# Kernel optimization log

Measured on AMD Instinct MI355X. Metric: run time of the kernel, lower is better.

## Reference

```python
import jax, jax.numpy as jnp
import numpy as np

NUM_USERS = 100000
NUM_ITEMS = 50000
N = NUM_USERS + NUM_ITEMS
E = 3000000
DIM = 64


def setup_inputs() -> dict:
    key = jax.random.key(0)
    ks = jax.random.split(key, 8)
    emb_users = 0.01 * jax.random.normal(ks[0], (NUM_USERS, DIM), dtype=jnp.float32)
    emb_items = 0.01 * jax.random.normal(ks[1], (NUM_ITEMS, DIM), dtype=jnp.float32)
    # GCNConv linear weights (bias separate, as in PyG: lin(bias=False) + bias param)
    s = 1.0 / np.sqrt(DIM)
    W1 = jax.random.uniform(ks[2], (DIM, DIM), jnp.float32, -s, s)
    b1 = jnp.zeros((DIM,), jnp.float32)
    W2 = jax.random.uniform(ks[3], (DIM, DIM), jnp.float32, -s, s)
    b2 = jnp.zeros((DIM,), jnp.float32)
    edge_index = jax.random.randint(ks[4], (2, E), 0, N, dtype=jnp.int64)
    edge_weight = jax.random.uniform(ks[5], (E,), jnp.float32)
    return {"emb_users": emb_users, "emb_items": emb_items,
            "W1": W1, "b1": b1, "W2": W2, "b2": b2,
            "edge_index": edge_index, "edge_weight": edge_weight}


def _gcn_conv(x, W, b, row, col):
    """PyG GCNConv with add_self_loops=True, improved=False, unit edge weights.
    out[i] = sum_{j->i} d_j^-1/2 d_i^-1/2 (x_j W) + d_i^-1 (x_i W) + b
    where d includes the self-loop (+1).
    """
    n = x.shape[0]
    xw = x @ W                                           # [N, D]
    deg = jax.ops.segment_sum(jnp.ones_like(row, dtype=x.dtype), col,
                              num_segments=n) + 1.0      # in-degree + self-loop
    dinv = jax.lax.rsqrt(deg)                            # [N]
    coef = dinv[row] * dinv[col]                         # [E]
    msg = xw[row] * coef[:, None]                        # gather + scale  [E, D]
    out = jax.ops.segment_sum(msg, col, num_segments=n)  # scatter-add     [N, D]
    out = out + xw * (dinv * dinv)[:, None]              # self-loop term
    return out + b


def reference(emb_users, emb_items, W1, b1, W2, b2, edge_index, edge_weight):
    # edge_weight is accepted by forward() but never passed to the GCN convs
    row, col = edge_index[0], edge_index[1]
    emb = jnp.concatenate([emb_users, emb_items], axis=0)  # [N, D]
    embs = [emb]
    for W, b in ((W1, b1), (W2, b2)):
        emb = _gcn_conv(emb, W, b, row, col)
        embs.append(emb)
        emb = jax.nn.relu(emb)
    return jnp.stack(embs)  # [num_layers+1, N, D]
```

## Files before the change

kernel.cpp:

```cpp
#include <hip/hip_runtime.h>
#include <hip/hip_fp16.h>

#define DIM 64
#define BPN 1024
#define ECHUNK 8192
#define MAXNB 160
#define BCAP 22528

typedef _Float16 f16x8 __attribute__((ext_vector_type(8)));
typedef float f32x4 __attribute__((ext_vector_type(4)));


__global__ __launch_bounds__(1024) void count_scatter_kernel(
    const int* __restrict__ row, const int* __restrict__ col,
    int* __restrict__ cursor_rel, int* __restrict__ packed, int E, int NB) {
  __shared__ int h[MAXNB];
  __shared__ int excl0[MAXNB];
  __shared__ int cur[MAXNB];
  __shared__ int gbase[MAXNB];
  __shared__ int wsum[16];
  __shared__ int woff[16];
  __shared__ int staging[ECHUNK];
  __shared__ unsigned short map[ECHUNK];
  const int tid = threadIdx.x;
  for (int t = tid; t < NB; t += blockDim.x) h[t] = 0;
  __syncthreads();
  int base = blockIdx.x * ECHUNK;
  int end = min(base + ECHUNK, E);
  int total = end - base;
  for (int e = base + tid; e < end; e += blockDim.x)
    atomicAdd(&h[col[e] >> 10], 1);
  __syncthreads();
  {
    const int lane = tid & 63, wid = tid >> 6;
    int v = (tid < NB) ? h[tid] : 0;
    int x = v;
#pragma unroll
    for (int d = 1; d < 64; d <<= 1) {
      int s = __shfl_up(x, d, 64);
      if (lane >= d) x += s;
    }
    if (lane == 63) wsum[wid] = x;
    __syncthreads();
    if (tid == 0) {
      int s = 0;
#pragma unroll
      for (int k = 0; k < 16; k++) { woff[k] = s; s += wsum[k]; }
    }
    __syncthreads();
    if (tid < NB) {
      int excl = woff[wid] + x - v;
      excl0[tid] = excl;
      cur[tid] = excl;
    }
  }
  __syncthreads();
  if (tid < NB) {
    if (h[tid] > 0)
      gbase[tid] = tid * BCAP + atomicAdd(&cursor_rel[tid], h[tid]);
    int s = excl0[tid], c = h[tid];
    for (int j = 0; j < c; j++) map[s + j] = (unsigned short)tid;
  }
  __syncthreads();
  for (int e = base + tid; e < end; e += blockDim.x) {
    int c = col[e];
    int b = c >> 10;
    int pos = atomicAdd(&cur[b], 1);
    staging[pos] = ((c & (BPN - 1)) << 18) | row[e];
  }
  __syncthreads();
  for (int idx = tid; idx < total; idx += blockDim.x) {
    int b = map[idx];
    packed[gbase[b] + idx - excl0[b]] = staging[idx];
  }
}

__global__ __launch_bounds__(256) void bucket_scan_kernel(
    const int* __restrict__ bucket_cnt, int* __restrict__ bucket_base,
    int* __restrict__ off, int NB, int N, int E) {
  __shared__ int wsum[4];
  __shared__ int woff[4];
  const int t = threadIdx.x;
  const int lane = t & 63, wid = t >> 6;
  int v = (t < NB) ? bucket_cnt[t] : 0;
  int x = v;
#pragma unroll
  for (int d = 1; d < 64; d <<= 1) {
    int s = __shfl_up(x, d, 64);
    if (lane >= d) x += s;
  }
  if (lane == 63) wsum[wid] = x;
  __syncthreads();
  if (t == 0) {
    int s = 0;
#pragma unroll
    for (int k = 0; k < 4; k++) { woff[k] = s; s += wsum[k]; }
  }
  __syncthreads();
  if (t < NB) bucket_base[t] = woff[wid] + x - v;
  if (t == 0) {
    bucket_base[NB] = woff[3] + wsum[3];
    off[N] = E;
  }
}

__global__ __launch_bounds__(1024) void bucket_csr_kernel(
    const int* __restrict__ packed, const int* __restrict__ bucket_base,
    int* __restrict__ perm_row, int* __restrict__ off, float* __restrict__ dinv, int N) {
  __shared__ int nh[BPN];
  __shared__ int ncur[BPN];
  __shared__ int wsum[16];
  __shared__ int woff[16];
  const int b = blockIdx.x;
  const int tid = threadIdx.x;
  const int rbase = b * BCAP;
  const int ebase = bucket_base[b];
  const int cnt = bucket_base[b + 1] - ebase;
  nh[tid] = 0;
  __syncthreads();
  for (int i = tid; i < cnt; i += 1024)
    atomicAdd(&nh[packed[rbase + i] >> 18], 1);
  __syncthreads();
  const int lane = tid & 63, wid = tid >> 6;
  int v = nh[tid], x = v;
#pragma unroll
  for (int d = 1; d < 64; d <<= 1) {
    int t = __shfl_up(x, d, 64);
    if (lane >= d) x += t;
  }
  if (lane == 63) wsum[wid] = x;
  __syncthreads();
  if (tid == 0) {
    int s = 0;
#pragma unroll
    for (int k = 0; k < 16; k++) { woff[k] = s; s += wsum[k]; }
  }
  __syncthreads();
  int excl = woff[wid] + x - v;
  ncur[tid] = excl;
  int node = b * BPN + tid;
  if (node < N) {
    off[node] = ebase + excl;
    dinv[node] = rsqrtf((float)v + 1.0f);
  }
  __syncthreads();
  for (int i = tid; i < cnt; i += 1024) {
    int p = packed[rbase + i];
    int local = p >> 18;
    int pos = atomicAdd(&ncur[local], 1);
    perm_row[ebase + pos] = p & 0x3FFFF;
  }
}

__global__ __launch_bounds__(256) void edge_coef_kernel(
    const int* __restrict__ perm_row, const float* __restrict__ dinv,
    int2* __restrict__ edata, int E) {
  int e = blockIdx.x * 256 + threadIdx.x;
  if (e >= E) return;
  int r = perm_row[e];
  edata[e] = make_int2(r, __float_as_int(dinv[r]));
}

__global__ __launch_bounds__(256) void xw_mfma_kernel(
    const float* __restrict__ xa, const float* __restrict__ xb,
    const float* __restrict__ W, float* __restrict__ out0,
    __half* __restrict__ xwh, int NU, int N, int do_relu) {
  __shared__ _Float16 Wt[64 * 72];
  for (int t = threadIdx.x; t < 4096; t += 256) {
    int k = t >> 6, n = t & 63;
    Wt[n * 72 + k] = (_Float16)W[t];
  }
  __syncthreads();
  const int lane = threadIdx.x & 63;
  const int wid = threadIdx.x >> 6;
  const int m = lane & 15;
  const int quad = lane >> 4;
  f16x8 bfrag[4][2];
#pragma unroll
  for (int c = 0; c < 4; c++)
#pragma unroll
    for (int s = 0; s < 2; s++)
      bfrag[c][s] = *(const f16x8*)&Wt[(c * 16 + m) * 72 + s * 32 + quad * 8];

  const int rbase = (blockIdx.x * 4 + wid) * 16;
  if (rbase >= N) return;
  const int r = rbase + m;
  const int rr = min(r, N - 1);
  const float* src = (xb == nullptr || rr < NU) ? xa + (size_t)rr * DIM
                                                : xb + (size_t)(rr - NU) * DIM;
  f16x8 afrag[2];
#pragma unroll
  for (int s = 0; s < 2; s++) {
    float4 u0 = *(const float4*)(src + s * 32 + quad * 8);
    float4 u1 = *(const float4*)(src + s * 32 + quad * 8 + 4);
    if (out0 != nullptr && r < N) {
      float4* o = (float4*)(out0 + (size_t)r * DIM);
      o[s * 8 + quad * 2] = u0;
      o[s * 8 + quad * 2 + 1] = u1;
    }
    if (do_relu) {
      u0.x = fmaxf(u0.x, 0.f); u0.y = fmaxf(u0.y, 0.f);
      u0.z = fmaxf(u0.z, 0.f); u0.w = fmaxf(u0.w, 0.f);
      u1.x = fmaxf(u1.x, 0.f); u1.y = fmaxf(u1.y, 0.f);
      u1.z = fmaxf(u1.z, 0.f); u1.w = fmaxf(u1.w, 0.f);
    }
    afrag[s][0] = (_Float16)u0.x; afrag[s][1] = (_Float16)u0.y;
    afrag[s][2] = (_Float16)u0.z; afrag[s][3] = (_Float16)u0.w;
    afrag[s][4] = (_Float16)u1.x; afrag[s][5] = (_Float16)u1.y;
    afrag[s][6] = (_Float16)u1.z; afrag[s][7] = (_Float16)u1.w;
  }
  f32x4 acc[4];
#pragma unroll
  for (int c = 0; c < 4; c++) {
    acc[c] = (f32x4){0.f, 0.f, 0.f, 0.f};
    acc[c] = __builtin_amdgcn_mfma_f32_16x16x32_f16(afrag[0], bfrag[c][0], acc[c], 0, 0, 0);
    acc[c] = __builtin_amdgcn_mfma_f32_16x16x32_f16(afrag[1], bfrag[c][1], acc[c], 0, 0, 0);
  }
#pragma unroll
  for (int reg = 0; reg < 4; reg++) {
    int orow = rbase + quad * 4 + reg;
    if (orow < N) {
      __half* dst = xwh + (size_t)orow * DIM + m;
#pragma unroll
      for (int c = 0; c < 4; c++)
        dst[c * 16] = __float2half(acc[c][reg]);
    }
  }
}

__global__ void aggregate_kernel(const __half* __restrict__ xwh, const int* __restrict__ off,
                                 const int2* __restrict__ edata, const float* __restrict__ dinv,
                                 const float* __restrict__ b, float* __restrict__ out,
                                 int nbase, int ncnt) {
  const int lane = threadIdx.x & 63;
  const int li = blockIdx.x * (blockDim.x >> 6) + (threadIdx.x >> 6);
  if (li >= ncnt) return;
  const int i = nbase + li;
  const int esel = lane >> 3;
  const int j = lane & 7;
  const float di = dinv[i];
  const float4* rows = (const float4*)xwh;
  float acc[8];
#pragma unroll
  for (int q = 0; q < 8; q++) acc[q] = 0.0f;
  if (esel == 0) {
    float4 f = rows[(size_t)i * 8 + j];
    const __half2* h = (const __half2*)&f;
#pragma unroll
    for (int q = 0; q < 4; q++) {
      float2 p = __half22float2(h[q]);
      acc[2 * q] = di * p.x;
      acc[2 * q + 1] = di * p.y;
    }
  }
  const int s0 = off[i], s1 = off[i + 1];
  const int last = s1 - 1;
  for (int k = s0; k < s1; k += 32) {
    const int e0 = k + esel, e1 = e0 + 8, e2 = e0 + 16, e3 = e0 + 24;
    int2 v0 = edata[min(e0, last)];
    int2 v1 = edata[min(e1, last)];
    int2 v2 = edata[min(e2, last)];
    int2 v3 = edata[min(e3, last)];
    float c0 = (e0 <= last) ? __int_as_float(v0.y) : 0.0f;
    float c1 = (e1 <= last) ? __int_as_float(v1.y) : 0.0f;
    float c2 = (e2 <= last) ? __int_as_float(v2.y) : 0.0f;
    float c3 = (e3 <= last) ? __int_as_float(v3.y) : 0.0f;
    float4 f0 = rows[(size_t)v0.x * 8 + j];
    float4 f1 = rows[(size_t)v1.x * 8 + j];
    float4 f2 = rows[(size_t)v2.x * 8 + j];
    float4 f3 = rows[(size_t)v3.x * 8 + j];
    const __half2* h0 = (const __half2*)&f0;
    const __half2* h1 = (const __half2*)&f1;
    const __half2* h2 = (const __half2*)&f2;
    const __half2* h3 = (const __half2*)&f3;
#pragma unroll
    for (int q = 0; q < 4; q++) {
      float2 p0 = __half22float2(h0[q]);
      acc[2 * q] += c0 * p0.x;
      acc[2 * q + 1] += c0 * p0.y;
    }
#pragma unroll
    for (int q = 0; q < 4; q++) {
      float2 p1 = __half22float2(h1[q]);
      acc[2 * q] += c1 * p1.x;
      acc[2 * q + 1] += c1 * p1.y;
    }
#pragma unroll
    for (int q = 0; q < 4; q++) {
      float2 p2 = __half22float2(h2[q]);
      acc[2 * q] += c2 * p2.x;
      acc[2 * q + 1] += c2 * p2.y;
    }
#pragma unroll
    for (int q = 0; q < 4; q++) {
      float2 p3 = __half22float2(h3[q]);
      acc[2 * q] += c3 * p3.x;
      acc[2 * q + 1] += c3 * p3.y;
    }
  }
#pragma unroll
  for (int q = 0; q < 8; q++) {
    acc[q] += __shfl_xor(acc[q], 8, 64);
    acc[q] += __shfl_xor(acc[q], 16, 64);
    acc[q] += __shfl_xor(acc[q], 32, 64);
  }
  if (esel == 0) {
    float4 b0 = ((const float4*)b)[2 * j];
    float4 b1 = ((const float4*)b)[2 * j + 1];
    float4* orow = (float4*)(out + (size_t)i * DIM);
    orow[2 * j] = make_float4(di * acc[0] + b0.x, di * acc[1] + b0.y,
                              di * acc[2] + b0.z, di * acc[3] + b0.w);
    orow[2 * j + 1] = make_float4(di * acc[4] + b1.x, di * acc[5] + b1.y,
                                  di * acc[6] + b1.z, di * acc[7] + b1.w);
  }
}

extern "C" void kernel_launch(void* const* d_in, const int* in_sizes, int n_in,
                              void* d_out, int out_size, void* d_ws, size_t ws_size,
                              hipStream_t stream) {
  const float* emb_users = (const float*)d_in[0];
  const float* emb_items = (const float*)d_in[1];
  const float* W1 = (const float*)d_in[2];
  const float* b1 = (const float*)d_in[3];
  const float* W2 = (const float*)d_in[4];
  const float* b2 = (const float*)d_in[5];
  const int* edge_index = (const int*)d_in[6];

  const int NU = in_sizes[0] / DIM;
  const int NI = in_sizes[1] / DIM;
  const int N = NU + NI;
  const int E = in_sizes[6] / 2;
  const int NB = (N + BPN - 1) / BPN;
  const int* row = edge_index;
  const int* col = edge_index + E;

  float* out = (float*)d_out;

  char* ws = (char*)d_ws;
  size_t o = 0;
  auto alloc = [&](size_t bytes) -> void* {
    o = (o + 255) & ~(size_t)255;
    void* p = ws + o;
    o += bytes;
    return p;
  };
  int* cursor_rel    = (int*)alloc((size_t)NB * 4);
  int* bucket_base   = (int*)alloc((size_t)(NB + 1) * 4);
  int* off           = (int*)alloc((size_t)(N + 1) * 4);
  float* dinv        = (float*)alloc((size_t)N * 4);
  int* perm_row      = (int*)alloc((size_t)E * 4);
  int2* edata        = (int2*)alloc((size_t)E * 8);
  __half* xwh        = (__half*)alloc((size_t)N * DIM * 2);
  int* packed        = (int*)xwh;
  (void)ws_size;

  const int nbE = (E + ECHUNK - 1) / ECHUNK;

  hipMemsetAsync(cursor_rel, 0, (size_t)NB * 4, stream);
  count_scatter_kernel<<<nbE, 1024, 0, stream>>>(row, col, cursor_rel, packed, E, NB);
  bucket_scan_kernel<<<1, 256, 0, stream>>>(cursor_rel, bucket_base, off, NB, N, E);
  bucket_csr_kernel<<<NB, 1024, 0, stream>>>(packed, bucket_base, perm_row, off, dinv, N);
  edge_coef_kernel<<<(E + 255) / 256, 256, 0, stream>>>(perm_row, dinv, edata, E);

  const int TB = 256;
  const int gx = (N + 63) / 64;
  const int NH = (N + 1) / 2;
  const int g1 = (NH + 3) / 4;
  const int g2 = (N - NH + 3) / 4;

  xw_mfma_kernel<<<gx, TB, 0, stream>>>(emb_users, emb_items, W1, out, xwh, NU, N, 0);
  aggregate_kernel<<<g1, TB, 0, stream>>>((const __half*)xwh, off, edata, dinv, b1,
                                          out + (size_t)N * DIM, 0, NH);
  aggregate_kernel<<<g2, TB, 0, stream>>>((const __half*)xwh, off, edata, dinv, b1,
                                          out + (size_t)N * DIM, NH, N - NH);

  xw_mfma_kernel<<<gx, TB, 0, stream>>>(out + (size_t)N * DIM, nullptr, W2, nullptr, xwh, N, N, 1);
  aggregate_kernel<<<g1, TB, 0, stream>>>((const __half*)xwh, off, edata, dinv, b2,
                                          out + (size_t)2 * N * DIM, 0, NH);
  aggregate_kernel<<<g2, TB, 0, stream>>>((const __half*)xwh, off, edata, dinv, b2,
                                          out + (size_t)2 * N * DIM, NH, N - NH);
}
```

Before: 398.6 us.

## Compute degrees in count pass, fuse edge coef into CSR build, merge aggregate launches

Degrees are now accumulated with global atomics during the count/scatter pass, and a small kernel turns them into dinv before CSR construction. The CSR kernel then writes the (row, dinv[row]) pair straight into edata, which removes the perm_row buffer and the separate edge_coef pass over E edges. The two half-range aggregate launches per layer become one launch each. The cost is 3M global atomics on deg and an extra small kernel plus memset size.

```diff
diff --git a/kernel.cpp b/kernel.cpp
--- a/kernel.cpp
+++ b/kernel.cpp
@@ -13,7 +13,8 @@
 
 __global__ __launch_bounds__(1024) void count_scatter_kernel(
     const int* __restrict__ row, const int* __restrict__ col,
-    int* __restrict__ cursor_rel, int* __restrict__ packed, int E, int NB) {
+    int* __restrict__ deg, int* __restrict__ cursor_rel,
+    int* __restrict__ packed, int E, int NB) {
   __shared__ int h[MAXNB];
   __shared__ int excl0[MAXNB];
   __shared__ int cur[MAXNB];
@@ -28,8 +29,11 @@
   int base = blockIdx.x * ECHUNK;
   int end = min(base + ECHUNK, E);
   int total = end - base;
-  for (int e = base + tid; e < end; e += blockDim.x)
-    atomicAdd(&h[col[e] >> 10], 1);
+  for (int e = base + tid; e < end; e += blockDim.x) {
+    int c = col[e];
+    atomicAdd(&h[c >> 10], 1);
+    atomicAdd(&deg[c], 1);
+  }
   __syncthreads();
   {
     const int lane = tid & 63, wid = tid >> 6;
@@ -73,6 +77,12 @@
     int b = map[idx];
     packed[gbase[b] + idx - excl0[b]] = staging[idx];
   }
+}
+
+__global__ __launch_bounds__(256) void dinv_kernel(
+    const int* __restrict__ deg, float* __restrict__ dinv, int N) {
+  int i = blockIdx.x * 256 + threadIdx.x;
+  if (i < N) dinv[i] = rsqrtf((float)deg[i] + 1.0f);
 }
 
 __global__ __launch_bounds__(256) void bucket_scan_kernel(
@@ -106,7 +116,8 @@
 
 __global__ __launch_bounds__(1024) void bucket_csr_kernel(
     const int* __restrict__ packed, const int* __restrict__ bucket_base,
-    int* __restrict__ perm_row, int* __restrict__ off, float* __restrict__ dinv, int N) {
+    const float* __restrict__ dinv, int2* __restrict__ edata,
+    int* __restrict__ off, int N) {
   __shared__ int nh[BPN];
   __shared__ int ncur[BPN];
   __shared__ int wsum[16];
@@ -139,26 +150,15 @@
   int excl = woff[wid] + x - v;
   ncur[tid] = excl;
   int node = b * BPN + tid;
-  if (node < N) {
-    off[node] = ebase + excl;
-    dinv[node] = rsqrtf((float)v + 1.0f);
-  }
+  if (node < N) off[node] = ebase + excl;
   __syncthreads();
   for (int i = tid; i < cnt; i += 1024) {
     int p = packed[rbase + i];
     int local = p >> 18;
     int pos = atomicAdd(&ncur[local], 1);
-    perm_row[ebase + pos] = p & 0x3FFFF;
-  }
-}
-
-__global__ __launch_bounds__(256) void edge_coef_kernel(
-    const int* __restrict__ perm_row, const float* __restrict__ dinv,
-    int2* __restrict__ edata, int E) {
-  int e = blockIdx.x * 256 + threadIdx.x;
-  if (e >= E) return;
-  int r = perm_row[e];
-  edata[e] = make_int2(r, __float_as_int(dinv[r]));
+    int r = p & 0x3FFFF;
+    edata[(size_t)(ebase + pos)] = make_int2(r, __float_as_int(dinv[r]));
+  }
 }
 
 __global__ __launch_bounds__(256) void xw_mfma_kernel(
@@ -230,12 +230,10 @@
 
 __global__ void aggregate_kernel(const __half* __restrict__ xwh, const int* __restrict__ off,
                                  const int2* __restrict__ edata, const float* __restrict__ dinv,
-                                 const float* __restrict__ b, float* __restrict__ out,
-                                 int nbase, int ncnt) {
+                                 const float* __restrict__ b, float* __restrict__ out, int n) {
   const int lane = threadIdx.x & 63;
-  const int li = blockIdx.x * (blockDim.x >> 6) + (threadIdx.x >> 6);
-  if (li >= ncnt) return;
-  const int i = nbase + li;
+  const int i = blockIdx.x * (blockDim.x >> 6) + (threadIdx.x >> 6);
+  if (i >= n) return;
   const int esel = lane >> 3;
   const int j = lane & 7;
   const float di = dinv[i];
@@ -345,10 +343,10 @@
     return p;
   };
   int* cursor_rel    = (int*)alloc((size_t)NB * 4);
+  int* deg           = (int*)alloc((size_t)N * 4);
   int* bucket_base   = (int*)alloc((size_t)(NB + 1) * 4);
   int* off           = (int*)alloc((size_t)(N + 1) * 4);
   float* dinv        = (float*)alloc((size_t)N * 4);
-  int* perm_row      = (int*)alloc((size_t)E * 4);
   int2* edata        = (int2*)alloc((size_t)E * 8);
   __half* xwh        = (__half*)alloc((size_t)N * DIM * 2);
   int* packed        = (int*)xwh;
@@ -356,27 +354,22 @@
 
   const int nbE = (E + ECHUNK - 1) / ECHUNK;
 
-  hipMemsetAsync(cursor_rel, 0, (size_t)NB * 4, stream);
-  count_scatter_kernel<<<nbE, 1024, 0, stream>>>(row, col, cursor_rel, packed, E, NB);
+  size_t zbytes = (size_t)((char*)(deg + N) - (char*)cursor_rel);
+  hipMemsetAsync(cursor_rel, 0, zbytes, stream);
+  count_scatter_kernel<<<nbE, 1024, 0, stream>>>(row, col, deg, cursor_rel, packed, E, NB);
+  dinv_kernel<<<(N + 255) / 256, 256, 0, stream>>>(deg, dinv, N);
   bucket_scan_kernel<<<1, 256, 0, stream>>>(cursor_rel, bucket_base, off, NB, N, E);
-  bucket_csr_kernel<<<NB, 1024, 0, stream>>>(packed, bucket_base, perm_row, off, dinv, N);
-  edge_coef_kernel<<<(E + 255) / 256, 256, 0, stream>>>(perm_row, dinv, edata, E);
+  bucket_csr_kernel<<<NB, 1024, 0, stream>>>(packed, bucket_base, dinv, edata, off, N);
 
   const int TB = 256;
   const int gx = (N + 63) / 64;
-  const int NH = (N + 1) / 2;
-  const int g1 = (NH + 3) / 4;
-  const int g2 = (N - NH + 3) / 4;
+  const int gr = (N + 3) / 4;
 
   xw_mfma_kernel<<<gx, TB, 0, stream>>>(emb_users, emb_items, W1, out, xwh, NU, N, 0);
-  aggregate_kernel<<<g1, TB, 0, stream>>>((const __half*)xwh, off, edata, dinv, b1,
-                                          out + (size_t)N * DIM, 0, NH);
-  aggregate_kernel<<<g2, TB, 0, stream>>>((const __half*)xwh, off, edata, dinv, b1,
-                                          out + (size_t)N * DIM, NH, N - NH);
+  aggregate_kernel<<<gr, TB, 0, stream>>>((const __half*)xwh, off, edata, dinv, b1,
+                                          out + (size_t)N * DIM, N);
 
   xw_mfma_kernel<<<gx, TB, 0, stream>>>(out + (size_t)N * DIM, nullptr, W2, nullptr, xwh, N, N, 1);
-  aggregate_kernel<<<g1, TB, 0, stream>>>((const __half*)xwh, off, edata, dinv, b2,
-                                          out + (size_t)2 * N * DIM, 0, NH);
-  aggregate_kernel<<<g2, TB, 0, stream>>>((const __half*)xwh, off, edata, dinv, b2,
-                                          out + (size_t)2 * N * DIM, NH, N - NH);
-}
+  aggregate_kernel<<<gr, TB, 0, stream>>>((const __half*)xwh, off, edata, dinv, b2,
+                                          out + (size_t)2 * N * DIM, N);
+}
```

After: 500.4 us. 25.5% more time.
